# Kernel tuning notes

Hardware: AMD Instinct MI355X
Metric: run time of the kernel (lower is better)

The kernel has to match this reference:

```python
import jax, jax.numpy as jnp
import numpy as np

N, E, DIN, D, H = 10000, 160000, 256, 64, 8
HC = D * H  # 512

def _p(key, shape, fan_in):
    return jax.random.normal(key, shape, dtype=jnp.float32) * (1.0 / np.sqrt(fan_in))

def setup_inputs() -> dict:
    key = jax.random.key(0)
    k = iter(jax.random.split(key, 64))
    inp = {}
    inp['x'] = jax.random.normal(next(k), (N, DIN), dtype=jnp.float32)
    inp['edge_index'] = jax.random.randint(next(k), (2, E), 0, N, dtype=jnp.int64)
    inp['Wp'] = _p(next(k), (DIN, D), DIN); inp['bp'] = jnp.zeros((D,), jnp.float32)
    # layer 0: in=D -> H*D
    for nm in ['Wq0', 'Wk0', 'Wv0', 'Ws0']:
        inp[nm] = _p(next(k), (D, HC), D)
    for nm in ['bq0', 'bk0', 'bv0', 'bs0']:
        inp[nm] = jnp.zeros((HC,), jnp.float32)
    # layers 1..4 stacked: in=HC -> HC
    for nm in ['Wq', 'Wk', 'Wv', 'Ws']:
        inp[nm] = _p(next(k), (4, HC, HC), HC)
    for nm in ['bq', 'bk', 'bv', 'bs']:
        inp[nm] = jnp.zeros((4, HC), jnp.float32)
    # final conv: in=HC -> D, heads=1, concat=False
    for nm in ['Wqf', 'Wkf', 'Wvf', 'Wsf']:
        inp[nm] = _p(next(k), (HC, D), HC)
    for nm in ['bqf', 'bkf', 'bvf', 'bsf']:
        inp[nm] = jnp.zeros((D,), jnp.float32)
    inp['Wc1'] = _p(next(k), (D, D // 2), D); inp['bc1'] = jnp.zeros((D // 2,), jnp.float32)
    inp['Wc2'] = _p(next(k), (D // 2, 2), D // 2); inp['bc2'] = jnp.zeros((2,), jnp.float32)
    return inp

def _tconv(x, src, dst, Wq, bq, Wk, bk, Wv, bv, Ws, bs, heads, concat):
    n = x.shape[0]
    c = Wq.shape[1] // heads
    q = (x @ Wq + bq).reshape(n, heads, c)
    kk = (x @ Wk + bk).reshape(n, heads, c)
    v = (x @ Wv + bv).reshape(n, heads, c)
    scale = 1.0 / jnp.sqrt(jnp.asarray(c, x.dtype))
    alpha = jnp.einsum('ehc,ehc->eh', q[dst], kk[src]) * scale  # [E,H]
    amax = jax.ops.segment_max(alpha, dst, num_segments=n)
    ex = jnp.exp(alpha - amax[dst])
    denom = jax.ops.segment_sum(ex, dst, num_segments=n)
    w = ex / denom[dst]  # segment softmax over incoming edges
    agg = jax.ops.segment_sum(w[:, :, None] * v[src], dst, num_segments=n)  # [N,H,C]
    skip = x @ Ws + bs
    if concat:
        return agg.reshape(n, heads * c) + skip
    return agg.mean(axis=1) + skip

def reference(x, edge_index, Wp, bp, Wq0, bq0, Wk0, bk0, Wv0, bv0, Ws0, bs0,
              Wq, bq, Wk, bk, Wv, bv, Ws, bs,
              Wqf, bqf, Wkf, bkf, Wvf, bvf, Wsf, bsf,
              Wc1, bc1, Wc2, bc2):
    src, dst = edge_index[0], edge_index[1]
    h = x @ Wp + bp
    h = jax.nn.relu(_tconv(h, src, dst, Wq0, bq0, Wk0, bk0, Wv0, bv0, Ws0, bs0, H, True))
    for l in range(4):
        h = jax.nn.relu(_tconv(h, src, dst, Wq[l], bq[l], Wk[l], bk[l], Wv[l], bv[l], Ws[l], bs[l], H, True))
    h = _tconv(h, src, dst, Wqf, bqf, Wkf, bkf, Wvf, bvf, Wsf, bsf, 1, False)
    g = h.mean(axis=0, keepdims=True)  # batch=None path: [1,D]
    logits = jax.nn.relu(g @ Wc1 + bc1) @ Wc2 + bc2
    return logits
```

## Files before the change

### kernel.cpp

```cpp
#include <hip/hip_runtime.h>
#include <hip/hip_bf16.h>
#include <cstddef>
#include <cstdint>

static inline int cdiv(int a, int b) { return (a + b - 1) / b; }

typedef short short8v __attribute__((ext_vector_type(8)));
typedef float float4v __attribute__((ext_vector_type(4)));

__device__ inline unsigned short f2b(float f) {
    union { float f; unsigned u; } x; x.f = f;
    unsigned u = x.u;
    return (unsigned short)((u + 0x7fff + ((u >> 16) & 1)) >> 16);
}

__device__ inline float lo2f(unsigned u) { union { unsigned x; float f; } c; c.x = u << 16; return c.f; }
__device__ inline float hi2f(unsigned u) { union { unsigned x; float f; } c; c.x = u & 0xffff0000u; return c.f; }
__device__ inline float b2f(unsigned short b) {
    union { unsigned u; float f; } x; x.u = ((unsigned)b) << 16;
    return x.f;
}

__device__ __forceinline__ void u4tof8(uint4 u, float* f) {
    f[0] = lo2f(u.x); f[1] = hi2f(u.x); f[2] = lo2f(u.y); f[3] = hi2f(u.y);
    f[4] = lo2f(u.z); f[5] = hi2f(u.z); f[6] = lo2f(u.w); f[7] = hi2f(u.w);
}

__device__ __forceinline__ void gload_lds16(const unsigned short* g, unsigned short* lds) {
    __builtin_amdgcn_global_load_lds(
        (const __attribute__((address_space(1))) unsigned int*)g,
        (__attribute__((address_space(3))) unsigned int*)lds, 16, 0, 0);
}


__global__ void count_kernel(const int* __restrict__ ei, int* __restrict__ indeg, int E) {
    int e = blockIdx.x * blockDim.x + threadIdx.x;
    if (e < E) atomicAdd(&indeg[ei[E + e]], 1);
}

__global__ void scan_kernel(const int* __restrict__ indeg, int* __restrict__ offs, int n) {
    __shared__ int tmp[1024];
    __shared__ int carry_s;
    int t = threadIdx.x;
    if (t == 0) { carry_s = 0; offs[0] = 0; }
    __syncthreads();
    for (int base = 0; base < n; base += 1024) {
        int i = base + t;
        int v = (i < n) ? indeg[i] : 0;
        tmp[t] = v;
        __syncthreads();
        for (int d = 1; d < 1024; d <<= 1) {
            int add = (t >= d) ? tmp[t - d] : 0;
            __syncthreads();
            tmp[t] += add;
            __syncthreads();
        }
        if (i < n) offs[i + 1] = carry_s + tmp[t];
        __syncthreads();
        if (t == 0) carry_s += tmp[1023];
        __syncthreads();
    }
}

__global__ void fill_kernel(const int* __restrict__ ei, const int* __restrict__ offs,
                            int* __restrict__ cursor, int* __restrict__ csrc, int E) {
    int e = blockIdx.x * blockDim.x + threadIdx.x;
    if (e < E) {
        int d = ei[E + e];
        int s = ei[e];
        int pos = atomicAdd(&cursor[d], 1);
        csrc[offs[d] + pos] = s;
    }
}


__global__ void f2b_kernel(const float* __restrict__ in, unsigned short* __restrict__ out, int n4) {
    int stride = gridDim.x * blockDim.x;
    for (int i = blockIdx.x * blockDim.x + threadIdx.x; i < n4; i += stride) {
        float4 v = reinterpret_cast<const float4*>(in)[i];
        ushort4 o;
        o.x = f2b(v.x); o.y = f2b(v.y); o.z = f2b(v.z); o.w = f2b(v.w);
        reinterpret_cast<ushort4*>(out)[i] = o;
    }
}

__global__ void transpose_b16_kernel(const float* __restrict__ Wq, const float* __restrict__ Wk,
                                     const float* __restrict__ Wv, const float* __restrict__ Ws,
                                     unsigned short* __restrict__ out) {
    const int K = 512, Nc = 512;
    int z = blockIdx.z;
    int which = z & 3;
    const float* W = (which == 0) ? Wq : (which == 1) ? Wk : (which == 2) ? Wv : Ws;
    W += (size_t)(z >> 2) * K * Nc;
    unsigned short* Wt = out + (size_t)z * K * Nc;
    __shared__ float t[32][33];
    int k0 = blockIdx.x * 32, c0 = blockIdx.y * 32;
    int tx = threadIdx.x, ty = threadIdx.y;
    #pragma unroll
    for (int i = 0; i < 32; i += 8) t[ty + i][tx] = W[(size_t)(k0 + ty + i) * Nc + c0 + tx];
    __syncthreads();
    #pragma unroll
    for (int i = 0; i < 32; i += 8) Wt[(size_t)(c0 + ty + i) * K + k0 + tx] = f2b(t[tx][ty + i]);
}

struct SmallT {
    const float* src[9];
    unsigned short* dst[9];
    int rows[9];
    int cols[9];
};

__global__ void transpose_small_kernel(SmallT p) {
    int mat = blockIdx.y;
    int rows = p.rows[mat], cols = p.cols[mat];
    int tilesC = cols >> 5;
    int tiles = (rows >> 5) * tilesC;
    if ((int)blockIdx.x >= tiles) return;
    int tr = blockIdx.x / tilesC, tc = blockIdx.x % tilesC;
    const float* src = p.src[mat];
    unsigned short* dst = p.dst[mat];
    __shared__ float t[32][33];
    int r0 = tr * 32, c0 = tc * 32;
    int tx = threadIdx.x, ty = threadIdx.y;
    #pragma unroll
    for (int i = 0; i < 32; i += 8) t[ty + i][tx] = src[(size_t)(r0 + ty + i) * cols + c0 + tx];
    __syncthreads();
    #pragma unroll
    for (int i = 0; i < 32; i += 8) dst[(size_t)(c0 + ty + i) * rows + r0 + tx] = f2b(t[tx][ty + i]);
}


struct GemmPtrs {
    const unsigned short* B[4];
    const float* bias[4];
    void* C[4];
    int bf16[4];
};

__global__ __launch_bounds__(256) void mfma_gemm4(const unsigned short* __restrict__ A,
                                                  GemmPtrs p, int M, int nb) {
    __shared__ unsigned short As[128 * 32];
    __shared__ unsigned short Bs[128 * 32];
    int i = blockIdx.x;
    int wk = (nb & 7) ? i : ((i & 7) * (nb >> 3) + (i >> 3));
    int xt = wk >> 4, yt = wk & 15;
    int row0 = xt * 128;
    int wsel = yt >> 2;
    int col0 = (yt & 3) * 128;
    const unsigned short* Bt = p.B[wsel];

    int tid = threadIdx.x;
    int lane = tid & 63;
    int w = tid >> 6;
    int wr = w >> 1, wc = w & 1;
    float4v acc[4][4] = {};

    int c0i = w * 2;
    int srow0 = c0i * 16 + (lane >> 2);
    int srow1 = srow0 + 16;
    int sslot0 = (lane & 3) ^ ((srow0 >> 1) & 3);
    int sslot1 = (lane & 3) ^ ((srow1 >> 1) & 3);

    const unsigned short* Abase = A + (size_t)row0 * 512;
    const unsigned short* Bbase = Bt + (size_t)col0 * 512;

    for (int k0 = 0; k0 < 512; k0 += 32) {
        gload_lds16(Abase + (size_t)srow0 * 512 + k0 + sslot0 * 8, &As[c0i * 512]);
        gload_lds16(Abase + (size_t)srow1 * 512 + k0 + sslot1 * 8, &As[(c0i + 1) * 512]);
        gload_lds16(Bbase + (size_t)srow0 * 512 + k0 + sslot0 * 8, &Bs[c0i * 512]);
        gload_lds16(Bbase + (size_t)srow1 * 512 + k0 + sslot1 * 8, &Bs[(c0i + 1) * 512]);
        __syncthreads();
        int r16 = lane & 15;
        int ks = lane >> 4;
        short8v af[4], bf[4];
        #pragma unroll
        for (int mi = 0; mi < 4; ++mi) {
            int row = wr * 64 + mi * 16 + r16;
            int slot = ks ^ ((row >> 1) & 3);
            af[mi] = *reinterpret_cast<const short8v*>(&As[row * 32 + slot * 8]);
        }
        #pragma unroll
        for (int nj = 0; nj < 4; ++nj) {
            int row = wc * 64 + nj * 16 + r16;
            int slot = ks ^ ((row >> 1) & 3);
            bf[nj] = *reinterpret_cast<const short8v*>(&Bs[row * 32 + slot * 8]);
        }
        #pragma unroll
        for (int mi = 0; mi < 4; ++mi)
            #pragma unroll
            for (int nj = 0; nj < 4; ++nj)
                acc[mi][nj] = __builtin_amdgcn_mfma_f32_16x16x32_bf16(af[mi], bf[nj], acc[mi][nj], 0, 0, 0);
        __syncthreads();
    }

    const float* bias = p.bias[wsel];
    int outbf = p.bf16[wsel];
    float* Cf = (float*)p.C[wsel];
    unsigned short* Cb = (unsigned short*)p.C[wsel];
    int crow_base = row0 + wr * 64 + (lane >> 4) * 4;
    int ccol_base = col0 + wc * 64 + (lane & 15);
    #pragma unroll
    for (int mi = 0; mi < 4; ++mi) {
        #pragma unroll
        for (int r = 0; r < 4; ++r) {
            int grow = crow_base + mi * 16 + r;
            if (grow >= M) continue;
            #pragma unroll
            for (int nj = 0; nj < 4; ++nj) {
                int gcol = ccol_base + nj * 16;
                float val = acc[mi][nj][r] + bias[gcol];
                if (outbf) Cb[(size_t)grow * 512 + gcol] = f2b(val);
                else       Cf[(size_t)grow * 512 + gcol] = val;
            }
        }
    }
}


__global__ __launch_bounds__(256) void mfma_flex(const unsigned short* __restrict__ A,
                                                 GemmPtrs p, int M, int K, int Nc) {
    __shared__ unsigned short As[128][40];
    __shared__ unsigned short Bs[64][40];
    int tid = threadIdx.x;
    int lane = tid & 63;
    int w = tid >> 6;
    int row0 = blockIdx.x * 128;
    int nb = Nc >> 6;
    int wsel = blockIdx.y / nb;
    int col0 = (blockIdx.y % nb) * 64;
    const unsigned short* Bt = p.B[wsel];

    float4v acc[2][4] = {};

    int ra = tid >> 1;
    int ca = (tid & 1) * 16;
    int rb = tid >> 2;
    int cb = (tid & 3) * 8;

    for (int k0 = 0; k0 < K; k0 += 32) {
        {
            int grow = row0 + ra;
            uint4 a0 = make_uint4(0u, 0u, 0u, 0u), a1 = make_uint4(0u, 0u, 0u, 0u);
            if (grow < M) {
                a0 = *reinterpret_cast<const uint4*>(&A[(size_t)grow * K + k0 + ca]);
                a1 = *reinterpret_cast<const uint4*>(&A[(size_t)grow * K + k0 + ca + 8]);
            }
            *reinterpret_cast<uint4*>(&As[ra][ca]) = a0;
            *reinterpret_cast<uint4*>(&As[ra][ca + 8]) = a1;
            uint4 bv = *reinterpret_cast<const uint4*>(&Bt[(size_t)(col0 + rb) * K + k0 + cb]);
            *reinterpret_cast<uint4*>(&Bs[rb][cb]) = bv;
        }
        __syncthreads();
        short8v af[2], bf[4];
        int r16 = lane & 15;
        int kc = (lane >> 4) * 8;
        #pragma unroll
        for (int mi = 0; mi < 2; ++mi)
            af[mi] = *reinterpret_cast<const short8v*>(&As[w * 32 + mi * 16 + r16][kc]);
        #pragma unroll
        for (int nj = 0; nj < 4; ++nj)
            bf[nj] = *reinterpret_cast<const short8v*>(&Bs[nj * 16 + r16][kc]);
        #pragma unroll
        for (int mi = 0; mi < 2; ++mi)
            #pragma unroll
            for (int nj = 0; nj < 4; ++nj)
                acc[mi][nj] = __builtin_amdgcn_mfma_f32_16x16x32_bf16(af[mi], bf[nj], acc[mi][nj], 0, 0, 0);
        __syncthreads();
    }

    const float* bias = p.bias[wsel];
    int outbf = p.bf16[wsel];
    float* Cf = (float*)p.C[wsel];
    unsigned short* Cb = (unsigned short*)p.C[wsel];
    int crow_base = row0 + w * 32 + (lane >> 4) * 4;
    int ccol_base = col0 + (lane & 15);
    #pragma unroll
    for (int mi = 0; mi < 2; ++mi) {
        #pragma unroll
        for (int r = 0; r < 4; ++r) {
            int grow = crow_base + mi * 16 + r;
            if (grow >= M) continue;
            #pragma unroll
            for (int nj = 0; nj < 4; ++nj) {
                int gcol = ccol_base + nj * 16;
                float val = acc[mi][nj][r] + bias[gcol];
                if (outbf) Cb[(size_t)grow * Nc + gcol] = f2b(val);
                else       Cf[(size_t)grow * Nc + gcol] = val;
            }
        }
    }
}


__global__ __launch_bounds__(256) void agg8_kernel(const unsigned short* __restrict__ q,
                                                   const unsigned short* __restrict__ kb,
                                                   const unsigned short* __restrict__ vb,
                                                   const unsigned short* __restrict__ skip,
                                                   const int* __restrict__ offs, const int* __restrict__ csrc,
                                                   unsigned short* __restrict__ outb, int N) {
    int lane = threadIdx.x & 63;
    int node = blockIdx.x * (blockDim.x >> 6) + (threadIdx.x >> 6);
    if (node >= N) return;

    unsigned co = (unsigned)lane * 8u;
    unsigned rbase = (unsigned)node * 512u + co;
    float qv[8];
    u4tof8(*reinterpret_cast<const uint4*>(&q[rbase]), qv);

    int e0 = offs[node], e1 = offs[node + 1];
    float m = -1e30f, wsum = 0.f;
    float accv[8] = {};
    const float SC = 0.125f * 1.4426950408889634f;

    int s = e0;
    for (; s + 4 <= e1; s += 4) {
        unsigned b0 = (unsigned)csrc[s] * 512u + co;
        unsigned b1 = (unsigned)csrc[s + 1] * 512u + co;
        unsigned b2 = (unsigned)csrc[s + 2] * 512u + co;
        unsigned b3 = (unsigned)csrc[s + 3] * 512u + co;
        uint4 k0 = *reinterpret_cast<const uint4*>(&kb[b0]);
        uint4 k1 = *reinterpret_cast<const uint4*>(&kb[b1]);
        uint4 k2 = *reinterpret_cast<const uint4*>(&kb[b2]);
        uint4 k3 = *reinterpret_cast<const uint4*>(&kb[b3]);
        uint4 v0 = *reinterpret_cast<const uint4*>(&vb[b0]);
        uint4 v1 = *reinterpret_cast<const uint4*>(&vb[b1]);
        uint4 v2 = *reinterpret_cast<const uint4*>(&vb[b2]);
        uint4 v3 = *reinterpret_cast<const uint4*>(&vb[b3]);
        float kk0[8], kk1[8], kk2[8], kk3[8];
        u4tof8(k0, kk0); u4tof8(k1, kk1); u4tof8(k2, kk2); u4tof8(k3, kk3);
        float d0 = 0.f, d1 = 0.f, d2 = 0.f, d3 = 0.f;
        #pragma unroll
        for (int j = 0; j < 8; ++j) {
            d0 += qv[j] * kk0[j]; d1 += qv[j] * kk1[j];
            d2 += qv[j] * kk2[j]; d3 += qv[j] * kk3[j];
        }
        d0 += __shfl_xor(d0, 1); d1 += __shfl_xor(d1, 1); d2 += __shfl_xor(d2, 1); d3 += __shfl_xor(d3, 1);
        d0 += __shfl_xor(d0, 2); d1 += __shfl_xor(d1, 2); d2 += __shfl_xor(d2, 2); d3 += __shfl_xor(d3, 2);
        d0 += __shfl_xor(d0, 4); d1 += __shfl_xor(d1, 4); d2 += __shfl_xor(d2, 4); d3 += __shfl_xor(d3, 4);
        float a0 = d0 * SC, a1 = d1 * SC, a2 = d2 * SC, a3 = d3 * SC;
        float am = fmaxf(fmaxf(a0, a1), fmaxf(a2, a3));
        if (__any(am > m + 8.f)) {
            float mnew = fmaxf(m, am);
            float corr = exp2f(m - mnew);
            wsum *= corr;
            #pragma unroll
            for (int j = 0; j < 8; ++j) accv[j] *= corr;
            m = mnew;
        }
        float x0 = exp2f(a0 - m);
        float x1 = exp2f(a1 - m);
        float x2 = exp2f(a2 - m);
        float x3 = exp2f(a3 - m);
        wsum += (x0 + x1) + (x2 + x3);
        float vv0[8], vv1[8], vv2[8], vv3[8];
        u4tof8(v0, vv0); u4tof8(v1, vv1); u4tof8(v2, vv2); u4tof8(v3, vv3);
        #pragma unroll
        for (int j = 0; j < 8; ++j)
            accv[j] += (x0 * vv0[j] + x1 * vv1[j]) + (x2 * vv2[j] + x3 * vv3[j]);
    }
    for (; s < e1; ++s) {
        unsigned b0 = (unsigned)csrc[s] * 512u + co;
        float kk0[8], vv0[8];
        u4tof8(*reinterpret_cast<const uint4*>(&kb[b0]), kk0);
        u4tof8(*reinterpret_cast<const uint4*>(&vb[b0]), vv0);
        float d0 = 0.f;
        #pragma unroll
        for (int j = 0; j < 8; ++j) d0 += qv[j] * kk0[j];
        d0 += __shfl_xor(d0, 1);
        d0 += __shfl_xor(d0, 2);
        d0 += __shfl_xor(d0, 4);
        float a0 = d0 * SC;
        if (__any(a0 > m + 8.f)) {
            float mnew = fmaxf(m, a0);
            float corr = exp2f(m - mnew);
            wsum *= corr;
            #pragma unroll
            for (int j = 0; j < 8; ++j) accv[j] *= corr;
            m = mnew;
        }
        float x0 = exp2f(a0 - m);
        wsum += x0;
        #pragma unroll
        for (int j = 0; j < 8; ++j) accv[j] += x0 * vv0[j];
    }

    float inv = (e1 > e0) ? (1.0f / wsum) : 0.f;
    float sk[8];
    u4tof8(*reinterpret_cast<const uint4*>(&skip[rbase]), sk);
    ushort4 o0, o1;
    o0.x = f2b(fmaxf(sk[0] + accv[0] * inv, 0.f));
    o0.y = f2b(fmaxf(sk[1] + accv[1] * inv, 0.f));
    o0.z = f2b(fmaxf(sk[2] + accv[2] * inv, 0.f));
    o0.w = f2b(fmaxf(sk[3] + accv[3] * inv, 0.f));
    o1.x = f2b(fmaxf(sk[4] + accv[4] * inv, 0.f));
    o1.y = f2b(fmaxf(sk[5] + accv[5] * inv, 0.f));
    o1.z = f2b(fmaxf(sk[6] + accv[6] * inv, 0.f));
    o1.w = f2b(fmaxf(sk[7] + accv[7] * inv, 0.f));
    *reinterpret_cast<ushort4*>(&outb[rbase]) = o0;
    *reinterpret_cast<ushort4*>(&outb[rbase + 4]) = o1;
}


__global__ __launch_bounds__(256) void aggf_kernel(const unsigned short* __restrict__ q,
                                                   const unsigned short* __restrict__ kb,
                                                   const unsigned short* __restrict__ vb,
                                                   const int* __restrict__ offs, const int* __restrict__ csrc,
                                                   float* __restrict__ out, int N) {
    const int HC = 64;
    int lane = threadIdx.x & 63;
    int node = blockIdx.x * (blockDim.x >> 6) + (threadIdx.x >> 6);
    if (node >= N) return;
    int g = lane >> 4;
    int r = lane & 15;

    unsigned qbase = (unsigned)node * 64u + 4u * r;
    ushort4 q4u = *reinterpret_cast<const ushort4*>(&q[qbase]);
    float q4[4] = {b2f(q4u.x), b2f(q4u.y), b2f(q4u.z), b2f(q4u.w)};

    int e0 = offs[node], e1 = offs[node + 1];
    float m = -3.4e38f, wsum = 0.f;
    float accv[4] = {0.f, 0.f, 0.f, 0.f};

    int nIt = (e1 - e0 + 3) >> 2;
    for (int it = 0; it < nIt; ++it) {
        int s = e0 + it * 4 + g;
        bool valid = s < e1;
        unsigned base = (unsigned)csrc[valid ? s : (e1 - 1)] * 64u + 4u * r;
        ushort4 k4 = *reinterpret_cast<const ushort4*>(&kb[base]);
        float d = q4[0] * b2f(k4.x) + q4[1] * b2f(k4.y) + q4[2] * b2f(k4.z) + q4[3] * b2f(k4.w);
        d += __shfl_xor(d, 1);
        d += __shfl_xor(d, 2);
        d += __shfl_xor(d, 4);
        d += __shfl_xor(d, 8);
        float alpha = valid ? d * 0.125f : -3.4e38f;
        float am = fmaxf(alpha, __shfl_xor(alpha, 16));
        am = fmaxf(am, __shfl_xor(am, 32));
        float mnew = fmaxf(m, am);
        float corr = __expf(m - mnew);
        float ex = __expf(alpha - mnew);
        ushort4 v4 = *reinterpret_cast<const ushort4*>(&vb[base]);
        wsum = wsum * corr + ex;
        accv[0] = accv[0] * corr + ex * b2f(v4.x);
        accv[1] = accv[1] * corr + ex * b2f(v4.y);
        accv[2] = accv[2] * corr + ex * b2f(v4.z);
        accv[3] = accv[3] * corr + ex * b2f(v4.w);
        m = mnew;
    }

    #pragma unroll
    for (int off = 16; off <= 32; off <<= 1) {
        wsum += __shfl_xor(wsum, off);
        #pragma unroll
        for (int j = 0; j < 4; ++j) accv[j] += __shfl_xor(accv[j], off);
    }

    if (g == 0) {
        float inv = (e1 > e0) ? (1.0f / wsum) : 0.f;
        float4 o = *reinterpret_cast<const float4*>(&out[qbase]);
        o.x += accv[0] * inv;
        o.y += accv[1] * inv;
        o.z += accv[2] * inv;
        o.w += accv[3] * inv;
        *reinterpret_cast<float4*>(&out[qbase]) = o;
    }
}


__global__ void pool_kernel(const float* __restrict__ hin, float* __restrict__ g, int N) {
    int dim = blockIdx.x;
    float s = 0.f;
    for (int i = threadIdx.x; i < N; i += blockDim.x) s += hin[(size_t)i * 64 + dim];
    __shared__ float red[256];
    red[threadIdx.x] = s;
    __syncthreads();
    for (int d = 128; d >= 1; d >>= 1) {
        if ((int)threadIdx.x < d) red[threadIdx.x] += red[threadIdx.x + d];
        __syncthreads();
    }
    if (threadIdx.x == 0) g[dim] = red[0] / (float)N;
}

__global__ void mlp_kernel(const float* __restrict__ g, const float* __restrict__ Wc1,
                           const float* __restrict__ bc1, const float* __restrict__ Wc2,
                           const float* __restrict__ bc2, float* __restrict__ out) {
    __shared__ float gs[64];
    __shared__ float h1[32];
    int t = threadIdx.x;
    if (t < 64) gs[t] = g[t];
    __syncthreads();
    if (t < 32) {
        float s = bc1[t];
        for (int i = 0; i < 64; ++i) s += gs[i] * Wc1[i * 32 + t];
        h1[t] = fmaxf(s, 0.f);
    }
    __syncthreads();
    if (t < 2) {
        float s = bc2[t];
        for (int i = 0; i < 32; ++i) s += h1[i] * Wc2[i * 2 + t];
        out[t] = s;
    }
}


extern "C" void kernel_launch(void* const* d_in, const int* in_sizes, int n_in,
                              void* d_out, int out_size, void* d_ws, size_t ws_size,
                              hipStream_t stream) {
    const float* x   = (const float*)d_in[0];
    const int*   ei  = (const int*)d_in[1];
    const float* Wp  = (const float*)d_in[2];
    const float* bp  = (const float*)d_in[3];
    const float* Wq0 = (const float*)d_in[4];
    const float* Wk0 = (const float*)d_in[5];
    const float* Wv0 = (const float*)d_in[6];
    const float* Ws0 = (const float*)d_in[7];
    const float* bq0 = (const float*)d_in[8];
    const float* bk0 = (const float*)d_in[9];
    const float* bv0 = (const float*)d_in[10];
    const float* bs0 = (const float*)d_in[11];
    const float* Wq  = (const float*)d_in[12];
    const float* Wk  = (const float*)d_in[13];
    const float* Wv  = (const float*)d_in[14];
    const float* Ws  = (const float*)d_in[15];
    const float* bq  = (const float*)d_in[16];
    const float* bk  = (const float*)d_in[17];
    const float* bv  = (const float*)d_in[18];
    const float* bs  = (const float*)d_in[19];
    const float* Wqf = (const float*)d_in[20];
    const float* Wkf = (const float*)d_in[21];
    const float* Wvf = (const float*)d_in[22];
    const float* Wsf = (const float*)d_in[23];
    const float* bqf = (const float*)d_in[24];
    const float* bkf = (const float*)d_in[25];
    const float* bvf = (const float*)d_in[26];
    const float* bsf = (const float*)d_in[27];
    const float* Wc1 = (const float*)d_in[28];
    const float* bc1 = (const float*)d_in[29];
    const float* Wc2 = (const float*)d_in[30];
    const float* bc2 = (const float*)d_in[31];

    const int N = in_sizes[0] / 256;
    const int E = in_sizes[1] / 2;
    const int HC = 512;

    size_t NB = (size_t)N * HC;
    const size_t WSMALL = 64 * 256 + 8 * 512 * 64;
    size_t need = 6 * NB * sizeof(unsigned short)
                + (size_t)16 * 512 * 512 * sizeof(unsigned short)
                + WSMALL * sizeof(unsigned short)
                + NB * sizeof(float)
                + (size_t)(2 * N + 1 + E) * sizeof(int)
                + 64 * sizeof(float) + 4096;
    if (ws_size < need) return;

    unsigned short* h0    = (unsigned short*)d_ws;
    unsigned short* h1    = h0 + NB;
    unsigned short* qb16  = h1 + NB;
    unsigned short* kb    = qb16 + NB;
    unsigned short* vb    = kb + NB;
    unsigned short* skipb = vb + NB;
    unsigned short* wt16  = skipb + NB;
    unsigned short* wsm   = wt16 + (size_t)16 * 512 * 512;
    uintptr_t pa = (uintptr_t)(wsm + WSMALL);
    pa = (pa + 255) & ~(uintptr_t)255;
    float* hf32 = (float*)pa;
    int* offs   = (int*)(hf32 + NB);
    int* cursor = offs + (N + 1);
    int* csrc   = cursor + N;
    float* gbuf = (float*)(csrc + E);
    unsigned short* xb = qb16;

    hipMemsetAsync(cursor, 0, sizeof(int) * N, stream);
    count_kernel<<<cdiv(E, 256), 256, 0, stream>>>(ei, cursor, E);
    scan_kernel<<<1, 1024, 0, stream>>>(cursor, offs, N);
    hipMemsetAsync(cursor, 0, sizeof(int) * N, stream);
    fill_kernel<<<cdiv(E, 256), 256, 0, stream>>>(ei, offs, cursor, csrc, E);

    transpose_b16_kernel<<<dim3(16, 16, 16), dim3(32, 8), 0, stream>>>(Wq, Wk, Wv, Ws, wt16);
    {
        SmallT st;
        unsigned short* wp_t = wsm;
        unsigned short* w0_t = wsm + 64 * 256;
        unsigned short* wf_t = w0_t + 4 * 512 * 64;
        st.src[0] = Wp;  st.dst[0] = wp_t; st.rows[0] = 256; st.cols[0] = 64;
        const float* w0s[4] = {Wq0, Wk0, Wv0, Ws0};
        const float* wfs[4] = {Wqf, Wkf, Wvf, Wsf};
        for (int i = 0; i < 4; ++i) {
            st.src[1 + i] = w0s[i]; st.dst[1 + i] = w0_t + i * 512 * 64;
            st.rows[1 + i] = 64; st.cols[1 + i] = 512;
            st.src[5 + i] = wfs[i]; st.dst[5 + i] = wf_t + i * 64 * 512;
            st.rows[5 + i] = 512; st.cols[5 + i] = 64;
        }
        transpose_small_kernel<<<dim3(32, 9), dim3(32, 8), 0, stream>>>(st);
    }

    f2b_kernel<<<1280, 256, 0, stream>>>(x, xb, N * 256 / 4);
    {
        GemmPtrs gp;
        for (int j = 0; j < 4; ++j) {
            gp.B[j] = wsm; gp.bias[j] = bp; gp.C[j] = h0; gp.bf16[j] = 1;
        }
        mfma_flex<<<dim3(cdiv(N, 128), 1), 256, 0, stream>>>(xb, gp, N, 256, 64);
    }

    {
        GemmPtrs gp;
        unsigned short* w0_t = wsm + 64 * 256;
        gp.B[0] = w0_t + 0 * 512 * 64; gp.bias[0] = bq0; gp.C[0] = qb16;  gp.bf16[0] = 1;
        gp.B[1] = w0_t + 1 * 512 * 64; gp.bias[1] = bk0; gp.C[1] = kb;    gp.bf16[1] = 1;
        gp.B[2] = w0_t + 2 * 512 * 64; gp.bias[2] = bv0; gp.C[2] = vb;    gp.bf16[2] = 1;
        gp.B[3] = w0_t + 3 * 512 * 64; gp.bias[3] = bs0; gp.C[3] = skipb; gp.bf16[3] = 1;
        mfma_flex<<<dim3(cdiv(N, 128), 4 * 8), 256, 0, stream>>>(h0, gp, N, 64, 512);
    }
    agg8_kernel<<<cdiv(N, 4), 256, 0, stream>>>(qb16, kb, vb, skipb, offs, csrc, h1, N);

    unsigned short* hcur = h1;
    unsigned short* hnext = h0;
    int gx = cdiv(N, 128);
    for (int l = 0; l < 4; ++l) {
        GemmPtrs gp;
        gp.B[0] = wt16 + (size_t)(l * 4 + 0) * 512 * 512;
        gp.B[1] = wt16 + (size_t)(l * 4 + 1) * 512 * 512;
        gp.B[2] = wt16 + (size_t)(l * 4 + 2) * 512 * 512;
        gp.B[3] = wt16 + (size_t)(l * 4 + 3) * 512 * 512;
        gp.bias[0] = bq + l * HC;
        gp.bias[1] = bk + l * HC;
        gp.bias[2] = bv + l * HC;
        gp.bias[3] = bs + l * HC;
        gp.C[0] = qb16; gp.C[1] = kb; gp.C[2] = vb; gp.C[3] = skipb;
        gp.bf16[0] = 1; gp.bf16[1] = 1; gp.bf16[2] = 1; gp.bf16[3] = 1;
        mfma_gemm4<<<gx * 16, 256, 0, stream>>>(hcur, gp, N, gx * 16);
        agg8_kernel<<<cdiv(N, 4), 256, 0, stream>>>(qb16, kb, vb, skipb, offs, csrc, hnext, N);
        { unsigned short* t = hcur; hcur = hnext; hnext = t; }
    }

    {
        GemmPtrs gp;
        unsigned short* wf_t = wsm + 64 * 256 + 4 * 512 * 64;
        gp.B[0] = wf_t + 0 * 64 * 512; gp.bias[0] = bqf; gp.C[0] = qb16; gp.bf16[0] = 1;
        gp.B[1] = wf_t + 1 * 64 * 512; gp.bias[1] = bkf; gp.C[1] = kb;   gp.bf16[1] = 1;
        gp.B[2] = wf_t + 2 * 64 * 512; gp.bias[2] = bvf; gp.C[2] = vb;   gp.bf16[2] = 1;
        gp.B[3] = wf_t + 3 * 64 * 512; gp.bias[3] = bsf; gp.C[3] = hf32; gp.bf16[3] = 0;
        mfma_flex<<<dim3(cdiv(N, 128), 4), 256, 0, stream>>>(hcur, gp, N, 512, 64);
    }
    aggf_kernel<<<cdiv(N, 4), 256, 0, stream>>>(qb16, kb, vb, offs, csrc, hf32, N);

    pool_kernel<<<64, 256, 0, stream>>>(hf32, gbuf, N);
    mlp_kernel<<<1, 64, 0, stream>>>(gbuf, Wc1, bc1, Wc2, bc2, (float*)d_out);
}
```

Before: 572.5 us.

## Triple-buffer GEMM K-loop with async LDS prefetch and parallelize CSR scan

The GEMM main loop now keeps three LDS stages, issuing global-to-LDS loads three K-tiles ahead and using explicit vmcnt waits with raw barriers, so memory latency overlaps MFMA work instead of stalling at each synchronization. Separately, the single-block serial CSR offset scan becomes a three-kernel block-parallel scan. The GEMM change triples LDS use per block, which may lower occupancy. The scan change adds two kernel launches and relies on manual waitcnt accounting being correct.

```diff
diff --git a/kernel.cpp b/kernel.cpp
--- a/kernel.cpp
+++ b/kernel.cpp
@@ -38,28 +38,34 @@
     if (e < E) atomicAdd(&indeg[ei[E + e]], 1);
 }
 
-__global__ void scan_kernel(const int* __restrict__ indeg, int* __restrict__ offs, int n) {
-    __shared__ int tmp[1024];
-    __shared__ int carry_s;
-    int t = threadIdx.x;
-    if (t == 0) { carry_s = 0; offs[0] = 0; }
+__global__ void scan1_kernel(const int* __restrict__ deg, int* __restrict__ offs,
+                             int* __restrict__ bsum, int n) {
+    __shared__ int tmp[256];
+    int i = blockIdx.x * 256 + threadIdx.x;
+    int v = (i < n) ? deg[i] : 0;
+    tmp[threadIdx.x] = v;
     __syncthreads();
-    for (int base = 0; base < n; base += 1024) {
-        int i = base + t;
-        int v = (i < n) ? indeg[i] : 0;
-        tmp[t] = v;
+    for (int d = 1; d < 256; d <<= 1) {
+        int a = (threadIdx.x >= (unsigned)d) ? tmp[threadIdx.x - d] : 0;
         __syncthreads();
-        for (int d = 1; d < 1024; d <<= 1) {
-            int add = (t >= d) ? tmp[t - d] : 0;
-            __syncthreads();
-            tmp[t] += add;
-            __syncthreads();
-        }
-        if (i < n) offs[i + 1] = carry_s + tmp[t];
+        tmp[threadIdx.x] += a;
         __syncthreads();
-        if (t == 0) carry_s += tmp[1023];
-        __syncthreads();
-    }
+    }
+    if (i < n) offs[i + 1] = tmp[threadIdx.x];
+    if (threadIdx.x == 255) bsum[blockIdx.x] = tmp[255];
+}
+
+__global__ void scan2_kernel(int* __restrict__ bsum, int* __restrict__ offs, int nb) {
+    if (threadIdx.x == 0) {
+        offs[0] = 0;
+        int base = 0;
+        for (int b = 0; b < nb; ++b) { int t = bsum[b]; bsum[b] = base; base += t; }
+    }
+}
+
+__global__ void scan3_kernel(int* __restrict__ offs, const int* __restrict__ bsum, int n) {
+    int i = blockIdx.x * 256 + threadIdx.x;
+    if (i < n) offs[i + 1] += bsum[blockIdx.x];
 }
 
 __global__ void fill_kernel(const int* __restrict__ ei, const int* __restrict__ offs,
@@ -139,8 +145,8 @@
 
 __global__ __launch_bounds__(256) void mfma_gemm4(const unsigned short* __restrict__ A,
                                                   GemmPtrs p, int M, int nb) {
-    __shared__ unsigned short As[128 * 32];
-    __shared__ unsigned short Bs[128 * 32];
+    __shared__ unsigned short As[3][128 * 32];
+    __shared__ unsigned short Bs[3][128 * 32];
     int i = blockIdx.x;
     int wk = (nb & 7) ? i : ((i & 7) * (nb >> 3) + (i >> 3));
     int xt = wk >> 4, yt = wk & 15;
@@ -161,36 +167,56 @@
     int sslot0 = (lane & 3) ^ ((srow0 >> 1) & 3);
     int sslot1 = (lane & 3) ^ ((srow1 >> 1) & 3);
 
-    const unsigned short* Abase = A + (size_t)row0 * 512;
-    const unsigned short* Bbase = Bt + (size_t)col0 * 512;
-
-    for (int k0 = 0; k0 < 512; k0 += 32) {
-        gload_lds16(Abase + (size_t)srow0 * 512 + k0 + sslot0 * 8, &As[c0i * 512]);
-        gload_lds16(Abase + (size_t)srow1 * 512 + k0 + sslot1 * 8, &As[(c0i + 1) * 512]);
-        gload_lds16(Bbase + (size_t)srow0 * 512 + k0 + sslot0 * 8, &Bs[c0i * 512]);
-        gload_lds16(Bbase + (size_t)srow1 * 512 + k0 + sslot1 * 8, &Bs[(c0i + 1) * 512]);
-        __syncthreads();
-        int r16 = lane & 15;
-        int ks = lane >> 4;
+    const unsigned short* Ag0 = A + (size_t)(row0 + srow0) * 512 + sslot0 * 8;
+    const unsigned short* Ag1 = A + (size_t)(row0 + srow1) * 512 + sslot1 * 8;
+    const unsigned short* Bg0 = Bt + (size_t)(col0 + srow0) * 512 + sslot0 * 8;
+    const unsigned short* Bg1 = Bt + (size_t)(col0 + srow1) * 512 + sslot1 * 8;
+
+    #pragma unroll
+    for (int t = 0; t < 3; ++t) {
+        gload_lds16(Ag0 + t * 32, &As[t][c0i * 512]);
+        gload_lds16(Ag1 + t * 32, &As[t][(c0i + 1) * 512]);
+        gload_lds16(Bg0 + t * 32, &Bs[t][c0i * 512]);
+        gload_lds16(Bg1 + t * 32, &Bs[t][(c0i + 1) * 512]);
+    }
+
+    int r16 = lane & 15;
+    int ks = lane >> 4;
+
+    #pragma unroll
+    for (int kt = 0; kt < 16; ++kt) {
+        if (kt <= 13)      { asm volatile("s_waitcnt vmcnt(8)" ::: "memory"); }
+        else if (kt == 14) { asm volatile("s_waitcnt vmcnt(4)" ::: "memory"); }
+        else               { asm volatile("s_waitcnt vmcnt(0)" ::: "memory"); }
+        __builtin_amdgcn_sched_barrier(0);
+        __builtin_amdgcn_s_barrier();
+        int buf = kt % 3;
         short8v af[4], bf[4];
         #pragma unroll
         for (int mi = 0; mi < 4; ++mi) {
             int row = wr * 64 + mi * 16 + r16;
             int slot = ks ^ ((row >> 1) & 3);
-            af[mi] = *reinterpret_cast<const short8v*>(&As[row * 32 + slot * 8]);
+            af[mi] = *reinterpret_cast<const short8v*>(&As[buf][row * 32 + slot * 8]);
         }
         #pragma unroll
         for (int nj = 0; nj < 4; ++nj) {
             int row = wc * 64 + nj * 16 + r16;
             int slot = ks ^ ((row >> 1) & 3);
-            bf[nj] = *reinterpret_cast<const short8v*>(&Bs[row * 32 + slot * 8]);
+            bf[nj] = *reinterpret_cast<const short8v*>(&Bs[buf][row * 32 + slot * 8]);
         }
         #pragma unroll
         for (int mi = 0; mi < 4; ++mi)
             #pragma unroll
             for (int nj = 0; nj < 4; ++nj)
                 acc[mi][nj] = __builtin_amdgcn_mfma_f32_16x16x32_bf16(af[mi], bf[nj], acc[mi][nj], 0, 0, 0);
-        __syncthreads();
+        __builtin_amdgcn_s_barrier();
+        if (kt <= 12) {
+            int nk = (kt + 3) * 32;
+            gload_lds16(Ag0 + nk, &As[buf][c0i * 512]);
+            gload_lds16(Ag1 + nk, &As[buf][(c0i + 1) * 512]);
+            gload_lds16(Bg0 + nk, &Bs[buf][c0i * 512]);
+            gload_lds16(Bg1 + nk, &Bs[buf][(c0i + 1) * 512]);
+        }
     }
 
     const float* bias = p.bias[wsel];
@@ -567,11 +593,16 @@
     int* cursor = offs + (N + 1);
     int* csrc   = cursor + N;
     float* gbuf = (float*)(csrc + E);
+    int*   bsum = (int*)(gbuf + 64);
     unsigned short* xb = qb16;
+
+    int nsb = cdiv(N, 256);
 
     hipMemsetAsync(cursor, 0, sizeof(int) * N, stream);
     count_kernel<<<cdiv(E, 256), 256, 0, stream>>>(ei, cursor, E);
-    scan_kernel<<<1, 1024, 0, stream>>>(cursor, offs, N);
+    scan1_kernel<<<nsb, 256, 0, stream>>>(cursor, offs, bsum, N);
+    scan2_kernel<<<1, 64, 0, stream>>>(bsum, offs, nsb);
+    scan3_kernel<<<nsb, 256, 0, stream>>>(offs, bsum, N);
     hipMemsetAsync(cursor, 0, sizeof(int) * N, stream);
     fill_kernel<<<cdiv(E, 256), 256, 0, stream>>>(ei, offs, cursor, csrc, E);
 
```

Measured after the change: 565.5 us, median of 2. About the same (-1.2%).
